# Performance work log

Hardware: AMD Instinct MI355X
Metric: run time of the kernel (lower is better)

Reference implementation:

```python
import jax, jax.numpy as jnp
import numpy as np

G, N, E, B = 4, 100000, 500000, 512
V, D, H, C = 50000, 300, 128, 20
NUM_HEADS, STEPS = 3, 2


def setup_inputs() -> dict:
    key = jax.random.key(0)
    ks = jax.random.split(key, 12)
    return {
        "node_indices": jax.random.randint(ks[0], (G, N), 0, V),
        "src": jax.random.randint(ks[1], (G, E), 0, N),
        "dst": jax.random.randint(ks[2], (G, E), 0, N),
        "node_graph_ids": jnp.sort(jax.random.randint(ks[3], (G, N), 0, B), axis=-1),
        "edge_weights": jax.random.uniform(ks[4], (G, E), dtype=jnp.float32),
        "emb_table": jax.random.normal(ks[5], (V, D), dtype=jnp.float32) * 0.1,
        "edge_params": jnp.ones((G,), dtype=jnp.float32),
        "W_proj": jax.random.normal(ks[6], (G, D, H), dtype=jnp.float32) / np.sqrt(D),
        "b_proj": jnp.zeros((G, H), dtype=jnp.float32),
        "W_cls": jax.random.normal(ks[7], (G, H, C), dtype=jnp.float32) / np.sqrt(H),
        "b_cls": jnp.zeros((G, C), dtype=jnp.float32),
        "W_fuse": jax.random.normal(ks[8], (NUM_HEADS, C, C, G), dtype=jnp.float32) / np.sqrt(C * G),
        "b_fuse": jnp.zeros((NUM_HEADS, C), dtype=jnp.float32),
    }


def _per_graph_logits(idx, s, d, gid, ew, emb_table, ep, Wp, bp, Wc, bc):
    # embedding lookup + input projection: [N, H]
    h = emb_table[idx] @ Wp + bp
    # graph_learning: relu(scalar * edge_weights)
    w = jax.nn.relu(ep * ew)  # [E]
    # in-degree for DGL mean reduce (0 in-edges -> 0 agg)
    deg = jax.ops.segment_sum(jnp.ones_like(ew), d, num_segments=N)
    inv_deg = jnp.where(deg > 0, 1.0 / deg, 0.0)[:, None]  # [N, 1]
    for _ in range(STEPS):
        msg = h[s] * w[:, None]                                   # gather-multiply [E, H]
        agg = jax.ops.segment_sum(msg, d, num_segments=N) * inv_deg  # scatter-mean [N, H]
        h = h + agg
    # dgl.mean_nodes: per-document mean of node features
    cnt = jax.ops.segment_sum(jnp.ones((N,), h.dtype), gid, num_segments=B)
    doc = jax.ops.segment_sum(h, gid, num_segments=B) / jnp.maximum(cnt, 1.0)[:, None]  # [B, H]
    # classify (dropout = identity in eval)
    return jax.nn.relu(doc) @ Wc + bc  # [B, C]


def reference(node_indices, src, dst, node_graph_ids, edge_weights, emb_table,
              edge_params, W_proj, b_proj, W_cls, b_cls, W_fuse, b_fuse):
    per_graph = jax.vmap(_per_graph_logits,
                         in_axes=(0, 0, 0, 0, 0, None, 0, 0, 0, 0, 0))
    logits = per_graph(node_indices, src, dst, node_graph_ids, edge_weights,
                       emb_table, edge_params, W_proj, b_proj, W_cls, b_cls)  # [G, B, C]
    stacked = jnp.transpose(logits, (1, 2, 0))  # [B, C_in, G] (Conv1d input, kernel=G)
    # Conv1d(out=C, in=C, k=G) per head, valid -> length 1, squeezed
    head_out = jnp.einsum('big,hoig->hbo', stacked, W_fuse) + b_fuse[:, None, :]  # [NH, B, C]
    fused_logits = head_out.mean(axis=0)  # [B, C]
    predictions = jax.nn.softmax(fused_logits, axis=-1)
    return predictions, fused_logits
```

## Files before the change

### kernel.cpp

```cpp
#include <hip/hip_runtime.h>

#define G_  4
#define N_  100000
#define E_  500000
#define B_  512
#define V_  50000
#define D_  300
#define H_  128
#define C_  20
#define NH_ 3

#define KP_  320
#define SCB_  512
#define NBLK_ ((N_ + SCB_ - 1) / SCB_)

typedef unsigned short ushort_t;
typedef __attribute__((ext_vector_type(8))) short bf16x8;
typedef __attribute__((ext_vector_type(4))) float f32x4;

__device__ __forceinline__ ushort_t f2bf(float f) {
    unsigned int x = __float_as_uint(f);
    unsigned int r = x + 0x7FFFu + ((x >> 16) & 1u);
    return (ushort_t)(r >> 16);
}

__device__ __forceinline__ int lower_bound_i(const int* __restrict__ a, int n, int v) {
    int lo = 0, hi = n;
    while (lo < hi) {
        int mid = (lo + hi) >> 1;
        if (a[mid] < v) lo = mid + 1; else hi = mid;
    }
    return lo;
}

__device__ __forceinline__ void unpack8(uint4 u, float* f) {
    f[0] = __uint_as_float((u.x & 0xFFFFu) << 16);
    f[1] = __uint_as_float(u.x & 0xFFFF0000u);
    f[2] = __uint_as_float((u.y & 0xFFFFu) << 16);
    f[3] = __uint_as_float(u.y & 0xFFFF0000u);
    f[4] = __uint_as_float((u.z & 0xFFFFu) << 16);
    f[5] = __uint_as_float(u.z & 0xFFFF0000u);
    f[6] = __uint_as_float((u.w & 0xFFFFu) << 16);
    f[7] = __uint_as_float(u.w & 0xFFFF0000u);
}

__global__ __launch_bounds__(256) void convert_w_kernel(
    const float* __restrict__ Wp,
    ushort_t* __restrict__ Wt)
{
    int flat = blockIdx.x * 256 + threadIdx.x;
    int g = flat / (H_ * KP_);
    int r = flat % (H_ * KP_);
    int n = r / KP_;
    int k = r % KP_;
    float v = (k < D_) ? Wp[((size_t)g * D_ + k) * H_ + n] : 0.f;
    Wt[flat] = f2bf(v);
}

__global__ __launch_bounds__(256) void mfma_gemm_kernel(
    const float* __restrict__ emb,
    const ushort_t* __restrict__ Wt,
    const float* __restrict__ bp,
    ushort_t* __restrict__ Ph)
{
    const int g    = blockIdx.x;
    const int row0 = blockIdx.y * 128;
    const int w    = threadIdx.x >> 6;
    const int l    = threadIdx.x & 63;
    const int l16  = l & 15;
    const int lk   = (l >> 4) * 8;

    const ushort_t* Wg = Wt + (size_t)g * H_ * KP_;
    ushort_t*       Pg = Ph + (size_t)g * V_ * H_;

    f32x4 acc[2][8];
#pragma unroll
    for (int m = 0; m < 2; ++m)
#pragma unroll
        for (int n = 0; n < 8; ++n) acc[m][n] = (f32x4){0.f, 0.f, 0.f, 0.f};

    const int wrow = row0 + w * 32;
    int arow[2];
    arow[0] = min(wrow + l16,      V_ - 1);
    arow[1] = min(wrow + 16 + l16, V_ - 1);

    for (int kp0 = 0; kp0 < KP_; kp0 += 32) {
        const int kb = kp0 + lk;

        bf16x8 a[2];
#pragma unroll
        for (int m = 0; m < 2; ++m) {
            float v[8];
            const float* ap = &emb[(size_t)arow[m] * D_ + kb];
            if (kb + 8 <= D_) {
                float4 x0 = *reinterpret_cast<const float4*>(ap);
                float4 x1 = *reinterpret_cast<const float4*>(ap + 4);
                v[0] = x0.x; v[1] = x0.y; v[2] = x0.z; v[3] = x0.w;
                v[4] = x1.x; v[5] = x1.y; v[6] = x1.z; v[7] = x1.w;
            } else {
#pragma unroll
                for (int j = 0; j < 8; ++j)
                    v[j] = (kb + j < D_) ? ap[j] : 0.f;
            }
#pragma unroll
            for (int j = 0; j < 8; ++j) a[m][j] = (short)f2bf(v[j]);
        }

        bf16x8 b[8];
#pragma unroll
        for (int n = 0; n < 8; ++n)
            b[n] = *reinterpret_cast<const bf16x8*>(&Wg[(size_t)(n * 16 + l16) * KP_ + kb]);

#pragma unroll
        for (int m = 0; m < 2; ++m)
#pragma unroll
            for (int n = 0; n < 8; ++n)
                acc[m][n] = __builtin_amdgcn_mfma_f32_16x16x32_bf16(
                    a[m], b[n], acc[m][n], 0, 0, 0);
    }

    const int rbase = (l >> 4) * 4;
#pragma unroll
    for (int n = 0; n < 8; ++n) {
        const int col  = n * 16 + l16;
        const float bv = bp[g * H_ + col];
#pragma unroll
        for (int m = 0; m < 2; ++m) {
#pragma unroll
            for (int r = 0; r < 4; ++r) {
                int row = wrow + m * 16 + rbase + r;
                if (row < V_)
                    Pg[(size_t)row * H_ + col] = f2bf(acc[m][n][r] + bv);
            }
        }
    }
}

__global__ __launch_bounds__(256) void deg_count_kernel(const int* __restrict__ dstA,
                                                        int* __restrict__ deg)
{
    const int g = blockIdx.y;
    int e = blockIdx.x * 256 + threadIdx.x;
    if (e < E_) atomicAdd(&deg[g * N_ + dstA[(size_t)g * E_ + e]], 1);
}

__global__ __launch_bounds__(512) void scan1_kernel(const int* __restrict__ deg,
                                                    int* __restrict__ bsum)
{
    __shared__ int sh[512];
    const int g = blockIdx.y, b = blockIdx.x, t = threadIdx.x;
    int i = b * SCB_ + t;
    sh[t] = (i < N_) ? deg[g * N_ + i] : 0;
    __syncthreads();
#pragma unroll
    for (int ofs = 256; ofs > 0; ofs >>= 1) {
        if (t < ofs) sh[t] += sh[t + ofs];
        __syncthreads();
    }
    if (t == 0) bsum[g * NBLK_ + b] = sh[0];
}

__global__ __launch_bounds__(256) void scan2_kernel(const int* __restrict__ bsum,
                                                    int* __restrict__ bpre,
                                                    int* __restrict__ off)
{
    __shared__ int sh[256];
    const int g = blockIdx.x, t = threadIdx.x;
    int v = (t < NBLK_) ? bsum[g * NBLK_ + t] : 0;
    sh[t] = v;
    __syncthreads();
#pragma unroll
    for (int ofs = 1; ofs < 256; ofs <<= 1) {
        int u = (t >= ofs) ? sh[t - ofs] : 0;
        __syncthreads();
        sh[t] += u;
        __syncthreads();
    }
    if (t < NBLK_) bpre[g * (NBLK_ + 1) + t + 1] = sh[t];
    if (t == 0) {
        bpre[g * (NBLK_ + 1)] = 0;
        off[(size_t)g * (N_ + 1) + N_] = sh[NBLK_ - 1];
    }
}

__global__ __launch_bounds__(512) void scan3_kernel(int* __restrict__ deg,
                                                    const int* __restrict__ bpre,
                                                    int* __restrict__ off)
{
    __shared__ int sh[512];
    const int g = blockIdx.y, b = blockIdx.x, t = threadIdx.x;
    int i = b * SCB_ + t;
    int v = (i < N_) ? deg[g * N_ + i] : 0;
    sh[t] = v;
    __syncthreads();
#pragma unroll
    for (int ofs = 1; ofs < 512; ofs <<= 1) {
        int u = (t >= ofs) ? sh[t - ofs] : 0;
        __syncthreads();
        sh[t] += u;
        __syncthreads();
    }
    if (i < N_) {
        off[(size_t)g * (N_ + 1) + i] = bpre[g * (NBLK_ + 1) + b] + sh[t] - v;
        deg[g * N_ + i] = 0;
    }
}

__global__ __launch_bounds__(256) void scatter_kernel(
    const int* __restrict__ srcA, const int* __restrict__ dstA,
    const float* __restrict__ ewA, const float* __restrict__ ep,
    const int* __restrict__ idxA, const int* __restrict__ off,
    int* __restrict__ cnt, int* __restrict__ csr_src,
    int* __restrict__ csr_vsrc, float* __restrict__ csr_coef)
{
    const int g = blockIdx.y;
    int e = blockIdx.x * 256 + threadIdx.x;
    if (e >= E_) return;
    int s = srcA[(size_t)g * E_ + e];
    int d = dstA[(size_t)g * E_ + e];
    int pos = off[(size_t)g * (N_ + 1) + d] + atomicAdd(&cnt[g * N_ + d], 1);
    csr_src[(size_t)g * E_ + pos]  = s;
    csr_vsrc[(size_t)g * E_ + pos] = idxA[(size_t)g * N_ + s];
    float w = ep[g] * ewA[(size_t)g * E_ + e];
    csr_coef[(size_t)g * E_ + pos] = fmaxf(w, 0.f);
}

__global__ __launch_bounds__(256) void prop1_kernel(
    const int* __restrict__ idx_g, const int* __restrict__ off,
    const int* __restrict__ csr_vsrc, const float* __restrict__ csr_coef,
    const ushort_t* __restrict__ Ph, ushort_t* __restrict__ hBh)
{
    const int n = blockIdx.x * 16 + (threadIdx.x >> 4);
    if (n >= N_) return;
    const int lane = threadIdx.x & 15;
    const int col  = lane * 8;

    const int lo = off[n], hi = off[n + 1];

    float sf[8];
    unpack8(*reinterpret_cast<const uint4*>(&Ph[(size_t)idx_g[n] * H_ + col]), sf);

    float acc[8];
#pragma unroll
    for (int j = 0; j < 8; ++j) acc[j] = 0.f;

    int i = lo;
    for (; i + 4 <= hi; i += 4) {
        int   s0 = csr_vsrc[i],     s1 = csr_vsrc[i + 1];
        int   s2 = csr_vsrc[i + 2], s3 = csr_vsrc[i + 3];
        float c0 = csr_coef[i],     c1 = csr_coef[i + 1];
        float c2 = csr_coef[i + 2], c3 = csr_coef[i + 3];
        uint4 u0 = *reinterpret_cast<const uint4*>(&Ph[(size_t)s0 * H_ + col]);
        uint4 u1 = *reinterpret_cast<const uint4*>(&Ph[(size_t)s1 * H_ + col]);
        uint4 u2 = *reinterpret_cast<const uint4*>(&Ph[(size_t)s2 * H_ + col]);
        uint4 u3 = *reinterpret_cast<const uint4*>(&Ph[(size_t)s3 * H_ + col]);
        float f0[8], f1[8], f2[8], f3[8];
        unpack8(u0, f0); unpack8(u1, f1); unpack8(u2, f2); unpack8(u3, f3);
#pragma unroll
        for (int j = 0; j < 8; ++j)
            acc[j] += c0 * f0[j] + c1 * f1[j] + c2 * f2[j] + c3 * f3[j];
    }
    for (; i < hi; ++i) {
        int   s = csr_vsrc[i];
        float c = csr_coef[i];
        float f[8];
        unpack8(*reinterpret_cast<const uint4*>(&Ph[(size_t)s * H_ + col]), f);
#pragma unroll
        for (int j = 0; j < 8; ++j) acc[j] += c * f[j];
    }

    const float inv = (hi > lo) ? 1.0f / (float)(hi - lo) : 0.f;
    ushort_t p[8];
#pragma unroll
    for (int j = 0; j < 8; ++j) p[j] = f2bf(sf[j] + inv * acc[j]);
    uint4 o;
    o.x = (unsigned)p[0] | ((unsigned)p[1] << 16);
    o.y = (unsigned)p[2] | ((unsigned)p[3] << 16);
    o.z = (unsigned)p[4] | ((unsigned)p[5] << 16);
    o.w = (unsigned)p[6] | ((unsigned)p[7] << 16);
    *reinterpret_cast<uint4*>(&hBh[(size_t)n * H_ + col]) = o;
}

__global__ __launch_bounds__(256) void prop2_kernel(
    const int* __restrict__ off, const int* __restrict__ csr_src,
    const float* __restrict__ csr_coef,
    const ushort_t* __restrict__ hBh, float* __restrict__ hA)
{
    const int n = blockIdx.x * 16 + (threadIdx.x >> 4);
    if (n >= N_) return;
    const int lane = threadIdx.x & 15;
    const int col  = lane * 8;

    const int lo = off[n], hi = off[n + 1];

    float sf[8];
    unpack8(*reinterpret_cast<const uint4*>(&hBh[(size_t)n * H_ + col]), sf);

    float acc[8];
#pragma unroll
    for (int j = 0; j < 8; ++j) acc[j] = 0.f;

    int i = lo;
    for (; i + 4 <= hi; i += 4) {
        int   s0 = csr_src[i],     s1 = csr_src[i + 1];
        int   s2 = csr_src[i + 2], s3 = csr_src[i + 3];
        float c0 = csr_coef[i],    c1 = csr_coef[i + 1];
        float c2 = csr_coef[i + 2], c3 = csr_coef[i + 3];
        uint4 u0 = *reinterpret_cast<const uint4*>(&hBh[(size_t)s0 * H_ + col]);
        uint4 u1 = *reinterpret_cast<const uint4*>(&hBh[(size_t)s1 * H_ + col]);
        uint4 u2 = *reinterpret_cast<const uint4*>(&hBh[(size_t)s2 * H_ + col]);
        uint4 u3 = *reinterpret_cast<const uint4*>(&hBh[(size_t)s3 * H_ + col]);
        float f0[8], f1[8], f2[8], f3[8];
        unpack8(u0, f0); unpack8(u1, f1); unpack8(u2, f2); unpack8(u3, f3);
#pragma unroll
        for (int j = 0; j < 8; ++j)
            acc[j] += c0 * f0[j] + c1 * f1[j] + c2 * f2[j] + c3 * f3[j];
    }
    for (; i < hi; ++i) {
        int   s = csr_src[i];
        float c = csr_coef[i];
        float f[8];
        unpack8(*reinterpret_cast<const uint4*>(&hBh[(size_t)s * H_ + col]), f);
#pragma unroll
        for (int j = 0; j < 8; ++j) acc[j] += c * f[j];
    }

    const float inv = (hi > lo) ? 1.0f / (float)(hi - lo) : 0.f;
    float4 o0, o1;
    o0.x = sf[0] + inv * acc[0]; o0.y = sf[1] + inv * acc[1];
    o0.z = sf[2] + inv * acc[2]; o0.w = sf[3] + inv * acc[3];
    o1.x = sf[4] + inv * acc[4]; o1.y = sf[5] + inv * acc[5];
    o1.z = sf[6] + inv * acc[6]; o1.w = sf[7] + inv * acc[7];
    *reinterpret_cast<float4*>(&hA[(size_t)n * H_ + col])     = o0;
    *reinterpret_cast<float4*>(&hA[(size_t)n * H_ + col + 4]) = o1;
}

__global__ __launch_bounds__(512) void doc_cls_kernel(
    const int* __restrict__ gid, const float* __restrict__ h,
    const float* __restrict__ Wc, const float* __restrict__ bc,
    float* __restrict__ logits)
{
    const int b   = blockIdx.x;
    const int tid = threadIdx.x;
    const int col = tid & 127;
    const int q   = tid >> 7;

    int lo = lower_bound_i(gid, N_, b);
    int hi = lower_bound_i(gid, N_, b + 1);

    float s = 0.f;
    for (int n = lo + q; n < hi; n += 4) s += h[(long)n * H_ + col];

    __shared__ float part[4][H_];
    part[q][col] = s;
    __syncthreads();

    __shared__ float sdoc[H_];
    if (tid < H_) {
        float tot = part[0][tid] + part[1][tid] + part[2][tid] + part[3][tid];
        float cnt = (float)(hi - lo);
        sdoc[tid] = fmaxf(tot / fmaxf(cnt, 1.0f), 0.f);
    }
    __syncthreads();

    if (tid < C_) {
        float acc = bc[tid];
#pragma unroll 8
        for (int hh = 0; hh < H_; ++hh) acc += sdoc[hh] * Wc[hh * C_ + tid];
        logits[b * C_ + tid] = acc;
    }
}

__global__ __launch_bounds__(64) void fuse_kernel(
    const float* __restrict__ logits,
    const float* __restrict__ Wf,
    const float* __restrict__ bf,
    float* __restrict__ out)
{
    const int b   = blockIdx.x;
    const int tid = threadIdx.x;

    __shared__ float s[C_ * G_];
    __shared__ float fl[C_];

    for (int t = tid; t < C_ * G_; t += 64) {
        int i = t >> 2, g = t & 3;
        s[t] = logits[((long)g * B_ + b) * C_ + i];
    }
    __syncthreads();

    if (tid < C_) {
        float acc = 0.f;
        for (int hd = 0; hd < NH_; ++hd) {
            float a = bf[hd * C_ + tid];
            const float* wrow = &Wf[((hd * C_ + tid) * C_) * G_];
#pragma unroll 5
            for (int i = 0; i < C_; ++i) {
#pragma unroll
                for (int g = 0; g < G_; ++g)
                    a += s[i * G_ + g] * wrow[i * G_ + g];
            }
            acc += a;
        }
        fl[tid] = acc * (1.0f / 3.0f);
    }
    __syncthreads();

    if (tid < C_) {
        float f = fl[tid];
        float m = -1e30f;
#pragma unroll
        for (int i = 0; i < C_; ++i) m = fmaxf(m, fl[i]);
        float ssum = 0.f;
#pragma unroll
        for (int i = 0; i < C_; ++i) ssum += expf(fl[i] - m);
        out[b * C_ + tid] = expf(f - m) / ssum;
        out[B_ * C_ + b * C_ + tid] = f;
    }
}

extern "C" void kernel_launch(void* const* d_in, const int* in_sizes, int n_in,
                              void* d_out, int out_size, void* d_ws, size_t ws_size,
                              hipStream_t stream)
{
    const int*   node_indices = (const int*)d_in[0];
    const int*   srcA         = (const int*)d_in[1];
    const int*   dstA         = (const int*)d_in[2];
    const int*   gidA         = (const int*)d_in[3];
    const float* ewA          = (const float*)d_in[4];
    const float* emb          = (const float*)d_in[5];
    const float* ep           = (const float*)d_in[6];
    const float* Wp           = (const float*)d_in[7];
    const float* bp           = (const float*)d_in[8];
    const float* Wc           = (const float*)d_in[9];
    const float* bc           = (const float*)d_in[10];
    const float* Wf           = (const float*)d_in[11];
    const float* bf           = (const float*)d_in[12];
    float*       out          = (float*)d_out;

    char* wp0 = (char*)d_ws;
    auto alloc = [&](size_t bytes) {
        void* r = (void*)wp0;
        wp0 += (bytes + 255) & ~(size_t)255;
        return r;
    };
    float*    hA       = (float*)   alloc((size_t)N_ * H_ * 4);
    ushort_t* hBh      = (ushort_t*)alloc((size_t)N_ * H_ * 2);
    float*    logits   = (float*)   alloc((size_t)G_ * B_ * C_ * 4);
    ushort_t* Wt       = (ushort_t*)alloc((size_t)G_ * H_ * KP_ * 2);
    int*      deg_i    = (int*)     alloc((size_t)G_ * N_ * 4);
    int*      off      = (int*)     alloc((size_t)G_ * (N_ + 1) * 4);
    int*      bsum     = (int*)     alloc((size_t)G_ * NBLK_ * 4);
    int*      bpre     = (int*)     alloc((size_t)G_ * (NBLK_ + 1) * 4);
    int*      csr_src  = (int*)     alloc((size_t)G_ * E_ * 4);
    int*      csr_vsrc = (int*)     alloc((size_t)G_ * E_ * 4);
    float*    csr_coef = (float*)   alloc((size_t)G_ * E_ * 4);

    const size_t pbytes = (size_t)V_ * H_ * 2;
    size_t used  = (size_t)(wp0 - (char*)d_ws);
    size_t avail = (ws_size > used) ? ws_size - used : 0;

    int ng;
    ushort_t* Ph;
    if (avail >= 4 * pbytes + 1024) {
        ng = 4; Ph = (ushort_t*)alloc(4 * pbytes);
    } else if (avail >= 2 * pbytes + 1024) {
        ng = 2; Ph = (ushort_t*)alloc(2 * pbytes);
    } else {
        ng = 1; Ph = (ushort_t*)hA;
    }

    convert_w_kernel<<<(G_ * H_ * KP_) / 256, 256, 0, stream>>>(Wp, Wt);

    hipMemsetAsync(deg_i, 0, (size_t)G_ * N_ * sizeof(int), stream);
    deg_count_kernel<<<dim3((E_ + 255) / 256, G_), 256, 0, stream>>>(dstA, deg_i);
    scan1_kernel<<<dim3(NBLK_, G_), 512, 0, stream>>>(deg_i, bsum);
    scan2_kernel<<<G_, 256, 0, stream>>>(bsum, bpre, off);
    scan3_kernel<<<dim3(NBLK_, G_), 512, 0, stream>>>(deg_i, bpre, off);
    scatter_kernel<<<dim3((E_ + 255) / 256, G_), 256, 0, stream>>>(
        srcA, dstA, ewA, ep, node_indices, off, deg_i, csr_src, csr_vsrc, csr_coef);

    for (int gbase = 0; gbase < G_; gbase += ng) {
        mfma_gemm_kernel<<<dim3(ng, (V_ + 127) / 128), 256, 0, stream>>>(
            emb, Wt + (size_t)gbase * H_ * KP_, bp + (size_t)gbase * H_, Ph);

        for (int gi = 0; gi < ng; ++gi) {
            const int g = gbase + gi;
            const int*      idx   = node_indices + (size_t)g * N_;
            const int*      gid   = gidA + (size_t)g * N_;
            const int*      off_g = off + (size_t)g * (N_ + 1);
            const ushort_t* Pg    = Ph + (size_t)gi * V_ * H_;

            prop1_kernel<<<(N_ + 15) / 16, 256, 0, stream>>>(
                idx, off_g, csr_vsrc + (size_t)g * E_, csr_coef + (size_t)g * E_,
                Pg, hBh);
            prop2_kernel<<<(N_ + 15) / 16, 256, 0, stream>>>(
                off_g, csr_src + (size_t)g * E_, csr_coef + (size_t)g * E_,
                hBh, hA);

            doc_cls_kernel<<<B_, 512, 0, stream>>>(
                gid, hA, Wc + (size_t)g * H_ * C_, bc + (size_t)g * C_,
                logits + (size_t)g * B_ * C_);
        }
    }

    fuse_kernel<<<B_, 64, 0, stream>>>(logits, Wf, bf, out);
}
```

Before: 642.4 us.

## Fuse second propagation with per-document pooling and pack CSR into int4 records

The second propagation step now reduces its output rows straight into per-document sums in shared memory and flushes them with atomics. This removes the fp32 hA write and the doc_cls re-read of 100000x128 floats per graph. Classification then runs once for all graphs in a single batched launch. The three separate CSR arrays (src, vsrc, coef) are packed into one 16-byte int4 record per edge, so each edge's fields come in one load. The cost is a padding word per edge, which raises edge-stream traffic, and nondeterministic float atomic accumulation order.

```diff
diff --git a/kernel.cpp b/kernel.cpp
--- a/kernel.cpp
+++ b/kernel.cpp
@@ -210,8 +210,7 @@
     const int* __restrict__ srcA, const int* __restrict__ dstA,
     const float* __restrict__ ewA, const float* __restrict__ ep,
     const int* __restrict__ idxA, const int* __restrict__ off,
-    int* __restrict__ cnt, int* __restrict__ csr_src,
-    int* __restrict__ csr_vsrc, float* __restrict__ csr_coef)
+    int* __restrict__ cnt, int4* __restrict__ csr4)
 {
     const int g = blockIdx.y;
     int e = blockIdx.x * 256 + threadIdx.x;
@@ -219,15 +218,14 @@
     int s = srcA[(size_t)g * E_ + e];
     int d = dstA[(size_t)g * E_ + e];
     int pos = off[(size_t)g * (N_ + 1) + d] + atomicAdd(&cnt[g * N_ + d], 1);
-    csr_src[(size_t)g * E_ + pos]  = s;
-    csr_vsrc[(size_t)g * E_ + pos] = idxA[(size_t)g * N_ + s];
     float w = ep[g] * ewA[(size_t)g * E_ + e];
-    csr_coef[(size_t)g * E_ + pos] = fmaxf(w, 0.f);
+    csr4[(size_t)g * E_ + pos] =
+        make_int4(s, idxA[(size_t)g * N_ + s], __float_as_int(fmaxf(w, 0.f)), 0);
 }
 
 __global__ __launch_bounds__(256) void prop1_kernel(
     const int* __restrict__ idx_g, const int* __restrict__ off,
-    const int* __restrict__ csr_vsrc, const float* __restrict__ csr_coef,
+    const int4* __restrict__ csr4,
     const ushort_t* __restrict__ Ph, ushort_t* __restrict__ hBh)
 {
     const int n = blockIdx.x * 16 + (threadIdx.x >> 4);
@@ -246,14 +244,14 @@
 
     int i = lo;
     for (; i + 4 <= hi; i += 4) {
-        int   s0 = csr_vsrc[i],     s1 = csr_vsrc[i + 1];
-        int   s2 = csr_vsrc[i + 2], s3 = csr_vsrc[i + 3];
-        float c0 = csr_coef[i],     c1 = csr_coef[i + 1];
-        float c2 = csr_coef[i + 2], c3 = csr_coef[i + 3];
-        uint4 u0 = *reinterpret_cast<const uint4*>(&Ph[(size_t)s0 * H_ + col]);
-        uint4 u1 = *reinterpret_cast<const uint4*>(&Ph[(size_t)s1 * H_ + col]);
-        uint4 u2 = *reinterpret_cast<const uint4*>(&Ph[(size_t)s2 * H_ + col]);
-        uint4 u3 = *reinterpret_cast<const uint4*>(&Ph[(size_t)s3 * H_ + col]);
+        int4 e0 = csr4[i],     e1 = csr4[i + 1];
+        int4 e2 = csr4[i + 2], e3 = csr4[i + 3];
+        float c0 = __int_as_float(e0.z), c1 = __int_as_float(e1.z);
+        float c2 = __int_as_float(e2.z), c3 = __int_as_float(e3.z);
+        uint4 u0 = *reinterpret_cast<const uint4*>(&Ph[(size_t)e0.y * H_ + col]);
+        uint4 u1 = *reinterpret_cast<const uint4*>(&Ph[(size_t)e1.y * H_ + col]);
+        uint4 u2 = *reinterpret_cast<const uint4*>(&Ph[(size_t)e2.y * H_ + col]);
+        uint4 u3 = *reinterpret_cast<const uint4*>(&Ph[(size_t)e3.y * H_ + col]);
         float f0[8], f1[8], f2[8], f3[8];
         unpack8(u0, f0); unpack8(u1, f1); unpack8(u2, f2); unpack8(u3, f3);
 #pragma unroll
@@ -261,10 +259,10 @@
             acc[j] += c0 * f0[j] + c1 * f1[j] + c2 * f2[j] + c3 * f3[j];
     }
     for (; i < hi; ++i) {
-        int   s = csr_vsrc[i];
-        float c = csr_coef[i];
+        int4 e0 = csr4[i];
+        float c = __int_as_float(e0.z);
         float f[8];
-        unpack8(*reinterpret_cast<const uint4*>(&Ph[(size_t)s * H_ + col]), f);
+        unpack8(*reinterpret_cast<const uint4*>(&Ph[(size_t)e0.y * H_ + col]), f);
 #pragma unroll
         for (int j = 0; j < 8; ++j) acc[j] += c * f[j];
     }
@@ -281,93 +279,110 @@
     *reinterpret_cast<uint4*>(&hBh[(size_t)n * H_ + col]) = o;
 }
 
-__global__ __launch_bounds__(256) void prop2_kernel(
-    const int* __restrict__ off, const int* __restrict__ csr_src,
-    const float* __restrict__ csr_coef,
-    const ushort_t* __restrict__ hBh, float* __restrict__ hA)
-{
-    const int n = blockIdx.x * 16 + (threadIdx.x >> 4);
-    if (n >= N_) return;
+__global__ __launch_bounds__(256) void prop2_fused_kernel(
+    const int* __restrict__ off, const int4* __restrict__ csr4,
+    const int* __restrict__ gid,
+    const ushort_t* __restrict__ hBh, float* __restrict__ docsum)
+{
+    const int nloc = threadIdx.x >> 4;
+    const int n    = blockIdx.x * 16 + nloc;
     const int lane = threadIdx.x & 15;
     const int col  = lane * 8;
 
-    const int lo = off[n], hi = off[n + 1];
-
-    float sf[8];
-    unpack8(*reinterpret_cast<const uint4*>(&hBh[(size_t)n * H_ + col]), sf);
-
-    float acc[8];
-#pragma unroll
-    for (int j = 0; j < 8; ++j) acc[j] = 0.f;
-
-    int i = lo;
-    for (; i + 4 <= hi; i += 4) {
-        int   s0 = csr_src[i],     s1 = csr_src[i + 1];
-        int   s2 = csr_src[i + 2], s3 = csr_src[i + 3];
-        float c0 = csr_coef[i],    c1 = csr_coef[i + 1];
-        float c2 = csr_coef[i + 2], c3 = csr_coef[i + 3];
-        uint4 u0 = *reinterpret_cast<const uint4*>(&hBh[(size_t)s0 * H_ + col]);
-        uint4 u1 = *reinterpret_cast<const uint4*>(&hBh[(size_t)s1 * H_ + col]);
-        uint4 u2 = *reinterpret_cast<const uint4*>(&hBh[(size_t)s2 * H_ + col]);
-        uint4 u3 = *reinterpret_cast<const uint4*>(&hBh[(size_t)s3 * H_ + col]);
-        float f0[8], f1[8], f2[8], f3[8];
-        unpack8(u0, f0); unpack8(u1, f1); unpack8(u2, f2); unpack8(u3, f3);
-#pragma unroll
-        for (int j = 0; j < 8; ++j)
-            acc[j] += c0 * f0[j] + c1 * f1[j] + c2 * f2[j] + c3 * f3[j];
-    }
-    for (; i < hi; ++i) {
-        int   s = csr_src[i];
-        float c = csr_coef[i];
-        float f[8];
-        unpack8(*reinterpret_cast<const uint4*>(&hBh[(size_t)s * H_ + col]), f);
-#pragma unroll
-        for (int j = 0; j < 8; ++j) acc[j] += c * f[j];
-    }
-
-    const float inv = (hi > lo) ? 1.0f / (float)(hi - lo) : 0.f;
-    float4 o0, o1;
-    o0.x = sf[0] + inv * acc[0]; o0.y = sf[1] + inv * acc[1];
-    o0.z = sf[2] + inv * acc[2]; o0.w = sf[3] + inv * acc[3];
-    o1.x = sf[4] + inv * acc[4]; o1.y = sf[5] + inv * acc[5];
-    o1.z = sf[6] + inv * acc[6]; o1.w = sf[7] + inv * acc[7];
-    *reinterpret_cast<float4*>(&hA[(size_t)n * H_ + col])     = o0;
-    *reinterpret_cast<float4*>(&hA[(size_t)n * H_ + col + 4]) = o1;
-}
-
-__global__ __launch_bounds__(512) void doc_cls_kernel(
-    const int* __restrict__ gid, const float* __restrict__ h,
+    __shared__ float sh[16][H_];
+    __shared__ int   shgid[16];
+
+    float o[8];
+    if (n < N_) {
+        const int lo = off[n], hi = off[n + 1];
+
+        float sf[8];
+        unpack8(*reinterpret_cast<const uint4*>(&hBh[(size_t)n * H_ + col]), sf);
+
+        float acc[8];
+#pragma unroll
+        for (int j = 0; j < 8; ++j) acc[j] = 0.f;
+
+        int i = lo;
+        for (; i + 4 <= hi; i += 4) {
+            int4 e0 = csr4[i],     e1 = csr4[i + 1];
+            int4 e2 = csr4[i + 2], e3 = csr4[i + 3];
+            float c0 = __int_as_float(e0.z), c1 = __int_as_float(e1.z);
+            float c2 = __int_as_float(e2.z), c3 = __int_as_float(e3.z);
+            uint4 u0 = *reinterpret_cast<const uint4*>(&hBh[(size_t)e0.x * H_ + col]);
+            uint4 u1 = *reinterpret_cast<const uint4*>(&hBh[(size_t)e1.x * H_ + col]);
+            uint4 u2 = *reinterpret_cast<const uint4*>(&hBh[(size_t)e2.x * H_ + col]);
+            uint4 u3 = *reinterpret_cast<const uint4*>(&hBh[(size_t)e3.x * H_ + col]);
+            float f0[8], f1[8], f2[8], f3[8];
+            unpack8(u0, f0); unpack8(u1, f1); unpack8(u2, f2); unpack8(u3, f3);
+#pragma unroll
+            for (int j = 0; j < 8; ++j)
+                acc[j] += c0 * f0[j] + c1 * f1[j] + c2 * f2[j] + c3 * f3[j];
+        }
+        for (; i < hi; ++i) {
+            int4 e0 = csr4[i];
+            float c = __int_as_float(e0.z);
+            float f[8];
+            unpack8(*reinterpret_cast<const uint4*>(&hBh[(size_t)e0.x * H_ + col]), f);
+#pragma unroll
+            for (int j = 0; j < 8; ++j) acc[j] += c * f[j];
+        }
+
+        const float inv = (hi > lo) ? 1.0f / (float)(hi - lo) : 0.f;
+#pragma unroll
+        for (int j = 0; j < 8; ++j) o[j] = sf[j] + inv * acc[j];
+        if (lane == 0) shgid[nloc] = gid[n];
+    } else {
+#pragma unroll
+        for (int j = 0; j < 8; ++j) o[j] = 0.f;
+        if (lane == 0) shgid[nloc] = -1;
+    }
+
+#pragma unroll
+    for (int j = 0; j < 8; ++j) sh[nloc][col + j] = o[j];
+    __syncthreads();
+
+    const int c  = threadIdx.x & 127;
+    const int q  = threadIdx.x >> 7;
+    const int n0 = q * 8;
+    float run = 0.f;
+    int rgid = shgid[n0];
+    for (int k = 0; k < 8; ++k) {
+        int gk = shgid[n0 + k];
+        if (gk != rgid) {
+            if (rgid >= 0) atomicAdd(&docsum[(size_t)rgid * H_ + c], run);
+            run = 0.f; rgid = gk;
+        }
+        run += sh[n0 + k][c];
+    }
+    if (rgid >= 0) atomicAdd(&docsum[(size_t)rgid * H_ + c], run);
+}
+
+__global__ __launch_bounds__(128) void cls_kernel(
+    const int* __restrict__ gidA, const float* __restrict__ docsum,
     const float* __restrict__ Wc, const float* __restrict__ bc,
     float* __restrict__ logits)
 {
     const int b   = blockIdx.x;
+    const int g   = blockIdx.y;
     const int tid = threadIdx.x;
-    const int col = tid & 127;
-    const int q   = tid >> 7;
+    const int* gid = gidA + (size_t)g * N_;
 
     int lo = lower_bound_i(gid, N_, b);
     int hi = lower_bound_i(gid, N_, b + 1);
-
-    float s = 0.f;
-    for (int n = lo + q; n < hi; n += 4) s += h[(long)n * H_ + col];
-
-    __shared__ float part[4][H_];
-    part[q][col] = s;
-    __syncthreads();
+    float cnt = (float)(hi - lo);
 
     __shared__ float sdoc[H_];
-    if (tid < H_) {
-        float tot = part[0][tid] + part[1][tid] + part[2][tid] + part[3][tid];
-        float cnt = (float)(hi - lo);
-        sdoc[tid] = fmaxf(tot / fmaxf(cnt, 1.0f), 0.f);
-    }
+    float dv = docsum[((size_t)g * B_ + b) * H_ + tid] / fmaxf(cnt, 1.0f);
+    sdoc[tid] = fmaxf(dv, 0.f);
     __syncthreads();
 
     if (tid < C_) {
-        float acc = bc[tid];
+        const float* Wcg = Wc + (size_t)g * H_ * C_;
+        float acc = bc[g * C_ + tid];
 #pragma unroll 8
-        for (int hh = 0; hh < H_; ++hh) acc += sdoc[hh] * Wc[hh * C_ + tid];
-        logits[b * C_ + tid] = acc;
+        for (int hh = 0; hh < H_; ++hh) acc += sdoc[hh] * Wcg[hh * C_ + tid];
+        logits[((size_t)g * B_ + b) * C_ + tid] = acc;
     }
 }
 
@@ -395,7 +410,7 @@
             float a = bf[hd * C_ + tid];
             const float* wrow = &Wf[((hd * C_ + tid) * C_) * G_];
 #pragma unroll 5
-            for (int i = 0; i < C_; ++i) {
+        for (int i = 0; i < C_; ++i) {
 #pragma unroll
                 for (int g = 0; g < G_; ++g)
                     a += s[i * G_ + g] * wrow[i * G_ + g];
@@ -444,33 +459,28 @@
         wp0 += (bytes + 255) & ~(size_t)255;
         return r;
     };
-    float*    hA       = (float*)   alloc((size_t)N_ * H_ * 4);
     ushort_t* hBh      = (ushort_t*)alloc((size_t)N_ * H_ * 2);
+    float*    docsum   = (float*)   alloc((size_t)G_ * B_ * H_ * 4);
     float*    logits   = (float*)   alloc((size_t)G_ * B_ * C_ * 4);
     ushort_t* Wt       = (ushort_t*)alloc((size_t)G_ * H_ * KP_ * 2);
     int*      deg_i    = (int*)     alloc((size_t)G_ * N_ * 4);
     int*      off      = (int*)     alloc((size_t)G_ * (N_ + 1) * 4);
     int*      bsum     = (int*)     alloc((size_t)G_ * NBLK_ * 4);
     int*      bpre     = (int*)     alloc((size_t)G_ * (NBLK_ + 1) * 4);
-    int*      csr_src  = (int*)     alloc((size_t)G_ * E_ * 4);
-    int*      csr_vsrc = (int*)     alloc((size_t)G_ * E_ * 4);
-    float*    csr_coef = (float*)   alloc((size_t)G_ * E_ * 4);
+    int4*     csr4     = (int4*)    alloc((size_t)G_ * E_ * 16);
 
     const size_t pbytes = (size_t)V_ * H_ * 2;
     size_t used  = (size_t)(wp0 - (char*)d_ws);
     size_t avail = (ws_size > used) ? ws_size - used : 0;
 
     int ng;
-    ushort_t* Ph;
-    if (avail >= 4 * pbytes + 1024) {
-        ng = 4; Ph = (ushort_t*)alloc(4 * pbytes);
-    } else if (avail >= 2 * pbytes + 1024) {
-        ng = 2; Ph = (ushort_t*)alloc(2 * pbytes);
-    } else {
-        ng = 1; Ph = (ushort_t*)hA;
-    }
+    if (avail >= 4 * pbytes + 1024)      ng = 4;
+    else if (avail >= 2 * pbytes + 1024) ng = 2;
+    else                                 ng = 1;
+    ushort_t* Ph = (ushort_t*)alloc((size_t)ng * pbytes);
 
     convert_w_kernel<<<(G_ * H_ * KP_) / 256, 256, 0, stream>>>(Wp, Wt);
+    hipMemsetAsync(docsum, 0, (size_t)G_ * B_ * H_ * sizeof(float), stream);
 
     hipMemsetAsync(deg_i, 0, (size_t)G_ * N_ * sizeof(int), stream);
     deg_count_kernel<<<dim3((E_ + 255) / 256, G_), 256, 0, stream>>>(dstA, deg_i);
@@ -478,7 +488,7 @@
     scan2_kernel<<<G_, 256, 0, stream>>>(bsum, bpre, off);
     scan3_kernel<<<dim3(NBLK_, G_), 512, 0, stream>>>(deg_i, bpre, off);
     scatter_kernel<<<dim3((E_ + 255) / 256, G_), 256, 0, stream>>>(
-        srcA, dstA, ewA, ep, node_indices, off, deg_i, csr_src, csr_vsrc, csr_coef);
+        srcA, dstA, ewA, ep, node_indices, off, deg_i, csr4);
 
     for (int gbase = 0; gbase < G_; gbase += ng) {
         mfma_gemm_kernel<<<dim3(ng, (V_ + 127) / 128), 256, 0, stream>>>(
@@ -489,20 +499,16 @@
             const int*      idx   = node_indices + (size_t)g * N_;
             const int*      gid   = gidA + (size_t)g * N_;
             const int*      off_g = off + (size_t)g * (N_ + 1);
+            const int4*     csr_g = csr4 + (size_t)g * E_;
             const ushort_t* Pg    = Ph + (size_t)gi * V_ * H_;
 
             prop1_kernel<<<(N_ + 15) / 16, 256, 0, stream>>>(
-                idx, off_g, csr_vsrc + (size_t)g * E_, csr_coef + (size_t)g * E_,
-                Pg, hBh);
-            prop2_kernel<<<(N_ + 15) / 16, 256, 0, stream>>>(
-                off_g, csr_src + (size_t)g * E_, csr_coef + (size_t)g * E_,
-                hBh, hA);
-
-            doc_cls_kernel<<<B_, 512, 0, stream>>>(
-                gid, hA, Wc + (size_t)g * H_ * C_, bc + (size_t)g * C_,
-                logits + (size_t)g * B_ * C_);
-        }
-    }
-
+                idx, off_g, csr_g, Pg, hBh);
+            prop2_fused_kernel<<<(N_ + 15) / 16, 256, 0, stream>>>(
+                off_g, csr_g, gid, hBh, docsum + (size_t)g * B_ * H_);
+        }
+    }
+
+    cls_kernel<<<dim3(B_, G_), 128, 0, stream>>>(gidA, docsum, Wc, bc, logits);
     fuse_kernel<<<B_, 64, 0, stream>>>(logits, Wf, bf, out);
 }
```

Result: faster. 548.8 us (-14.6%).
